# Kernel tuning notes

Hardware: AMD Instinct MI355X
Metric: run time of the kernel (lower is better)

The kernel has to match this reference:

```python
import jax, jax.numpy as jnp
import numpy as np

N_NODES = 100000
N_EDGES = 1600000
IN_FT = 128
OUT_FT = 128


def setup_inputs() -> dict:
    key = jax.random.key(0)
    k1, k2, k3, k4, k5, k6 = jax.random.split(key, 6)
    stdv = 1.0 / np.sqrt(OUT_FT)
    x = jax.random.normal(k1, (N_NODES, IN_FT), dtype=jnp.float32)
    edge_rows = jax.random.randint(k2, (N_EDGES,), 0, N_NODES, dtype=jnp.int32)
    edge_cols = jax.random.randint(k3, (N_EDGES,), 0, N_NODES, dtype=jnp.int32)
    # normalized adjacency values (positive, like D^-1 A)
    edge_vals = jax.random.uniform(k4, (N_EDGES,), dtype=jnp.float32)
    W = jax.random.uniform(k5, (IN_FT, OUT_FT), dtype=jnp.float32, minval=-stdv, maxval=stdv)
    b = jax.random.uniform(k6, (OUT_FT,), dtype=jnp.float32, minval=-stdv, maxval=stdv)
    return {"x": x, "edge_rows": edge_rows, "edge_cols": edge_cols,
            "edge_vals": edge_vals, "W": W, "b": b}


def reference(x, edge_rows, edge_cols, edge_vals, W, b):
    # dense projection + bias: [N, out_ft]
    h = x @ W + b
    # SpMM: out[r] = sum_e vals[e] * h[cols[e]] for edges with rows[e] == r
    msgs = edge_vals[:, None] * h[edge_cols]          # [E, out_ft]
    out = jax.ops.segment_sum(msgs, edge_rows, num_segments=N_NODES)
    return jax.nn.relu(out)
```

## Files before the change

### kernel.cpp

```cpp
#include <hip/hip_runtime.h>

#define N_NODES 100000
#define N_EDGES 1600000
#define FT 128

#define NBUCK 391
#define EPB 4096
#define NBLKP ((N_EDGES + EPB - 1) / EPB)
#define CAP 6144

#define OFF_H 0
#define OFF_BUCKETED 25600000
#define OFF_BLKHIST 38400000
#define OFF_BTOT 39011524
#define OFF_BBASE 39013088
#define WS_NEEDED 39014656

typedef __attribute__((ext_vector_type(8))) short bf16x8;
typedef __attribute__((ext_vector_type(4))) float f32x4;

static __device__ __forceinline__ ushort f2bf(float f) {
  const unsigned u = __float_as_uint(f);
  return (ushort)((u + 0x7FFF + ((u >> 16) & 1)) >> 16);
}
static __device__ __forceinline__ float bf2f(ushort s) {
  return __uint_as_float((unsigned)s << 16);
}

__global__ __launch_bounds__(256) void gemm_bias_kernel(
    const float* __restrict__ x,
    const float* __restrict__ W,
    const float* __restrict__ b,
    ushort* __restrict__ h) {
  __shared__ __align__(16) ushort whi[16384];
  __shared__ __align__(16) ushort wlo[16384];

  const int tid = threadIdx.x;

  for (int idx = tid; idx < 16384; idx += 256) {
    const int k = idx >> 7;
    const int col = idx & 127;
    const float wv = W[idx];
    const ushort hi = f2bf(wv);
    const ushort lo = f2bf(wv - bf2f(hi));
    const int lane_ = (((k >> 3) & 3) << 4) | (col & 15);
    const int pos = ((((k >> 5) << 3) + (col >> 4)) * 64 + lane_) * 8 + (k & 7);
    whi[pos] = hi;
    wlo[pos] = lo;
  }
  __syncthreads();

  const int w = tid >> 6;
  const int lane = tid & 63;
  const int r0 = blockIdx.x * 256 + w * 64;
  const int arow = lane & 15;
  const int kgrp = (lane >> 4) << 3;

  float bias_v[8];
#pragma unroll
  for (int ct = 0; ct < 8; ++ct) bias_v[ct] = b[ct * 16 + (lane & 15)];

  f32x4 acc[4][8];
#pragma unroll
  for (int rf = 0; rf < 4; ++rf)
#pragma unroll
    for (int ct = 0; ct < 8; ++ct) acc[rf][ct] = (f32x4){0.f, 0.f, 0.f, 0.f};

#pragma unroll
  for (int ks = 0; ks < 4; ++ks) {
    bf16x8 afr[4];
#pragma unroll
    for (int rf = 0; rf < 4; ++rf) {
      int r = r0 + rf * 16 + arow;
      r = (r < N_NODES) ? r : (N_NODES - 1);
      const float* xp = x + (size_t)r * FT + ks * 32 + kgrp;
      const float4 u0 = *(const float4*)xp;
      const float4 u1 = *(const float4*)(xp + 4);
      bf16x8 a;
      a[0] = (short)f2bf(u0.x);
      a[1] = (short)f2bf(u0.y);
      a[2] = (short)f2bf(u0.z);
      a[3] = (short)f2bf(u0.w);
      a[4] = (short)f2bf(u1.x);
      a[5] = (short)f2bf(u1.y);
      a[6] = (short)f2bf(u1.z);
      a[7] = (short)f2bf(u1.w);
      afr[rf] = a;
    }
#pragma unroll
    for (int ct = 0; ct < 8; ++ct) {
      const int fo = ((ks * 8 + ct) * 64 + lane) * 8;
      const bf16x8 bh = *(const bf16x8*)&whi[fo];
      const bf16x8 bl = *(const bf16x8*)&wlo[fo];
#pragma unroll
      for (int rf = 0; rf < 4; ++rf) {
        acc[rf][ct] = __builtin_amdgcn_mfma_f32_16x16x32_bf16(
            afr[rf], bh, acc[rf][ct], 0, 0, 0);
        acc[rf][ct] = __builtin_amdgcn_mfma_f32_16x16x32_bf16(
            afr[rf], bl, acc[rf][ct], 0, 0, 0);
      }
    }
  }

  const int crow0 = (lane >> 4) << 2;
  const int ccol = lane & 15;
#pragma unroll
  for (int rf = 0; rf < 4; ++rf) {
#pragma unroll
    for (int ct = 0; ct < 8; ++ct) {
      const int col = ct * 16 + ccol;
#pragma unroll
      for (int i = 0; i < 4; ++i) {
        const int row = r0 + rf * 16 + crow0 + i;
        if (row < N_NODES)
          h[(size_t)row * FT + col] = f2bf(acc[rf][ct][i] + bias_v[ct]);
      }
    }
  }
}

__global__ __launch_bounds__(256) void partA_kernel(
    const int* __restrict__ erows, int* __restrict__ blkhist) {
  __shared__ int cnt[NBUCK];
  const int tid = threadIdx.x;
  for (int j = tid; j < NBUCK; j += 256) cnt[j] = 0;
  __syncthreads();

  const int base4 = blockIdx.x * (EPB / 4);
#pragma unroll
  for (int it = 0; it < EPB / 4 / 256; ++it) {
    const int idx4 = base4 + it * 256 + tid;
    if (idx4 < N_EDGES / 4) {
      const int4 r = ((const int4*)erows)[idx4];
      atomicAdd(&cnt[r.x >> 8], 1);
      atomicAdd(&cnt[r.y >> 8], 1);
      atomicAdd(&cnt[r.z >> 8], 1);
      atomicAdd(&cnt[r.w >> 8], 1);
    }
  }
  __syncthreads();
  int* dst = blkhist + (size_t)blockIdx.x * NBUCK;
  for (int j = tid; j < NBUCK; j += 256) dst[j] = cnt[j];
}

__global__ __launch_bounds__(512) void partB1_kernel(
    int* __restrict__ blkhist, int* __restrict__ btot) {
  __shared__ int ps[512];
  const int b = blockIdx.x;
  const int t = threadIdx.x;
  int v = 0;
  if (t < NBLKP) v = blkhist[(size_t)t * NBUCK + b];
  ps[t] = v;
  __syncthreads();
#pragma unroll
  for (int d = 1; d < 512; d <<= 1) {
    const int u = (t >= d) ? ps[t - d] : 0;
    __syncthreads();
    ps[t] += u;
    __syncthreads();
  }
  if (t < NBLKP) blkhist[(size_t)t * NBUCK + b] = ps[t] - v;
  if (t == NBLKP - 1) btot[b] = ps[t];
}

__global__ __launch_bounds__(512) void partB2_kernel(
    const int* __restrict__ btot, int* __restrict__ bucket_base) {
  __shared__ int ps[512];
  const int t = threadIdx.x;
  int v = 0;
  if (t < NBUCK) v = btot[t];
  ps[t] = v;
  __syncthreads();
#pragma unroll
  for (int d = 1; d < 512; d <<= 1) {
    const int u = (t >= d) ? ps[t - d] : 0;
    __syncthreads();
    ps[t] += u;
    __syncthreads();
  }
  if (t < NBUCK) bucket_base[t] = ps[t] - v;
  if (t == NBUCK - 1) bucket_base[NBUCK] = ps[t];
}

__global__ __launch_bounds__(256) void partC_kernel(
    const int* __restrict__ erows,
    const int* __restrict__ ecols,
    const float* __restrict__ evals,
    const int* __restrict__ blkhist,
    const int* __restrict__ bucket_base,
    int2* __restrict__ bucketed) {
  __shared__ int cur[NBUCK];
  const int tid = threadIdx.x;
  const int* src = blkhist + (size_t)blockIdx.x * NBUCK;
  for (int j = tid; j < NBUCK; j += 256) cur[j] = src[j] + bucket_base[j];
  __syncthreads();

  const int base4 = blockIdx.x * (EPB / 4);
#pragma unroll
  for (int it = 0; it < EPB / 4 / 256; ++it) {
    const int idx4 = base4 + it * 256 + tid;
    if (idx4 < N_EDGES / 4) {
      const int4 r = ((const int4*)erows)[idx4];
      const int4 c = ((const int4*)ecols)[idx4];
      const float4 v = ((const float4*)evals)[idx4];
      int p;
      p = atomicAdd(&cur[r.x >> 8], 1);
      bucketed[p] = (int2){((r.x & 255) << 24) | c.x, __float_as_int(v.x)};
      p = atomicAdd(&cur[r.y >> 8], 1);
      bucketed[p] = (int2){((r.y & 255) << 24) | c.y, __float_as_int(v.y)};
      p = atomicAdd(&cur[r.z >> 8], 1);
      bucketed[p] = (int2){((r.z & 255) << 24) | c.z, __float_as_int(v.z)};
      p = atomicAdd(&cur[r.w >> 8], 1);
      bucketed[p] = (int2){((r.w & 255) << 24) | c.w, __float_as_int(v.w)};
    }
  }
}

__global__ __launch_bounds__(512) void spmm_bucket_kernel(
    const int2* __restrict__ bucketed,
    const int* __restrict__ bucket_base,
    const ushort* __restrict__ h,
    float* __restrict__ out) {
  __shared__ int2 eds[CAP];
  __shared__ int cnt[256];
  __shared__ int pos[256];
  __shared__ int cur[256];
  const int b = blockIdx.x;
  const int t = threadIdx.x;
  const int beg = bucket_base[b];
  const int end = bucket_base[b + 1];
  const int n = end - beg;
  const int m = (n < CAP) ? n : CAP;

  if (t < 256) cnt[t] = 0;
  __syncthreads();

  for (int i = t; i < m; i += 512)
    atomicAdd(&cnt[((unsigned)bucketed[beg + i].x) >> 24], 1);
  __syncthreads();

  if (t < 256) pos[t] = cnt[t];
  __syncthreads();
#pragma unroll
  for (int d = 1; d < 256; d <<= 1) {
    int u = 0;
    if (t < 256 && t >= d) u = pos[t - d];
    __syncthreads();
    if (t < 256) pos[t] += u;
    __syncthreads();
  }
  if (t < 256) {
    const int excl = pos[t] - cnt[t];
    pos[t] = excl;
    cur[t] = excl;
  }
  __syncthreads();

  for (int i = t; i < m; i += 512) {
    const int2 rec = bucketed[beg + i];
    const int r8 = ((unsigned)rec.x) >> 24;
    const int p = atomicAdd(&cur[r8], 1);
    eds[p] = (int2){rec.x & 0x00FFFFFF, rec.y};
  }
  __syncthreads();

  const int g = t >> 5;
  const int lane = t & 31;
  const int j = lane * 4;

  for (int rr = 0; rr < 16; ++rr) {
    const int r = rr * 16 + g;
    const int row = b * 256 + r;
    const int rbeg = pos[r];
    const int rend = cur[r];

    float a0 = 0.f, a1 = 0.f, a2 = 0.f, a3 = 0.f;
    int e = rbeg;
    for (; e + 3 < rend; e += 4) {
      const int2 p0 = eds[e];
      const int2 p1 = eds[e + 1];
      const int2 p2 = eds[e + 2];
      const int2 p3 = eds[e + 3];
      const ushort4 q0 = *(const ushort4*)(h + (size_t)p0.x * FT + j);
      const ushort4 q1 = *(const ushort4*)(h + (size_t)p1.x * FT + j);
      const ushort4 q2 = *(const ushort4*)(h + (size_t)p2.x * FT + j);
      const ushort4 q3 = *(const ushort4*)(h + (size_t)p3.x * FT + j);
      const float v0 = __int_as_float(p0.y);
      const float v1 = __int_as_float(p1.y);
      const float v2 = __int_as_float(p2.y);
      const float v3 = __int_as_float(p3.y);
      a0 = fmaf(v0, bf2f(q0.x), a0);
      a1 = fmaf(v0, bf2f(q0.y), a1);
      a2 = fmaf(v0, bf2f(q0.z), a2);
      a3 = fmaf(v0, bf2f(q0.w), a3);
      a0 = fmaf(v1, bf2f(q1.x), a0);
      a1 = fmaf(v1, bf2f(q1.y), a1);
      a2 = fmaf(v1, bf2f(q1.z), a2);
      a3 = fmaf(v1, bf2f(q1.w), a3);
      a0 = fmaf(v2, bf2f(q2.x), a0);
      a1 = fmaf(v2, bf2f(q2.y), a1);
      a2 = fmaf(v2, bf2f(q2.z), a2);
      a3 = fmaf(v2, bf2f(q2.w), a3);
      a0 = fmaf(v3, bf2f(q3.x), a0);
      a1 = fmaf(v3, bf2f(q3.y), a1);
      a2 = fmaf(v3, bf2f(q3.z), a2);
      a3 = fmaf(v3, bf2f(q3.w), a3);
    }
    for (; e < rend; ++e) {
      const int2 p0 = eds[e];
      const float v0 = __int_as_float(p0.y);
      const ushort4 q0 = *(const ushort4*)(h + (size_t)p0.x * FT + j);
      a0 = fmaf(v0, bf2f(q0.x), a0);
      a1 = fmaf(v0, bf2f(q0.y), a1);
      a2 = fmaf(v0, bf2f(q0.z), a2);
      a3 = fmaf(v0, bf2f(q0.w), a3);
    }
    if (n > CAP) {
      for (int i = beg + CAP; i < end; ++i) {
        const int2 rec = bucketed[i];
        if ((int)(((unsigned)rec.x) >> 24) == r) {
          const float v0 = __int_as_float(rec.y);
          const ushort4 q0 =
              *(const ushort4*)(h + (size_t)(rec.x & 0x00FFFFFF) * FT + j);
          a0 = fmaf(v0, bf2f(q0.x), a0);
          a1 = fmaf(v0, bf2f(q0.y), a1);
          a2 = fmaf(v0, bf2f(q0.z), a2);
          a3 = fmaf(v0, bf2f(q0.w), a3);
        }
      }
    }

    if (row < N_NODES) {
      float4 o;
      o.x = fmaxf(a0, 0.f);
      o.y = fmaxf(a1, 0.f);
      o.z = fmaxf(a2, 0.f);
      o.w = fmaxf(a3, 0.f);
      *(float4*)(out + (size_t)row * FT + j) = o;
    }
  }
}

__global__ __launch_bounds__(256) void edge_scatter_kernel(
    const int* __restrict__ erows,
    const int* __restrict__ ecols,
    const float* __restrict__ evals,
    const ushort* __restrict__ h,
    float* out) {
  const int tid = threadIdx.x;
  const int e = blockIdx.x * 8 + (tid >> 5);
  if (e >= N_EDGES) return;
  const int r = erows[e];
  const int c = ecols[e];
  const float v = evals[e];
  const int j = (tid & 31) * 4;
  const ushort4 q = *(const ushort4*)(h + (size_t)c * FT + j);
  float* op = out + (size_t)r * FT + j;
  atomicAdd(op + 0, v * bf2f(q.x));
  atomicAdd(op + 1, v * bf2f(q.y));
  atomicAdd(op + 2, v * bf2f(q.z));
  atomicAdd(op + 3, v * bf2f(q.w));
}

__global__ __launch_bounds__(256) void relu_kernel(float* out, int n4) {
  const int i = blockIdx.x * blockDim.x + threadIdx.x;
  if (i < n4) {
    float4 v = ((float4*)out)[i];
    v.x = fmaxf(v.x, 0.f);
    v.y = fmaxf(v.y, 0.f);
    v.z = fmaxf(v.z, 0.f);
    v.w = fmaxf(v.w, 0.f);
    ((float4*)out)[i] = v;
  }
}

extern "C" void kernel_launch(void* const* d_in, const int* in_sizes, int n_in,
                              void* d_out, int out_size, void* d_ws, size_t ws_size,
                              hipStream_t stream) {
  const float* x = (const float*)d_in[0];
  const int* erows = (const int*)d_in[1];
  const int* ecols = (const int*)d_in[2];
  const float* evals = (const float*)d_in[3];
  const float* W = (const float*)d_in[4];
  const float* b = (const float*)d_in[5];
  float* out = (float*)d_out;

  char* ws = (char*)d_ws;
  ushort* h = (ushort*)(ws + OFF_H);

  gemm_bias_kernel<<<(N_NODES + 255) / 256, 256, 0, stream>>>(x, W, b, h);

  if (ws_size >= (size_t)WS_NEEDED) {
    int2* bucketed = (int2*)(ws + OFF_BUCKETED);
    int* blkhist = (int*)(ws + OFF_BLKHIST);
    int* btot = (int*)(ws + OFF_BTOT);
    int* bucket_base = (int*)(ws + OFF_BBASE);

    partA_kernel<<<NBLKP, 256, 0, stream>>>(erows, blkhist);
    partB1_kernel<<<NBUCK, 512, 0, stream>>>(blkhist, btot);
    partB2_kernel<<<1, 512, 0, stream>>>(btot, bucket_base);
    partC_kernel<<<NBLKP, 256, 0, stream>>>(erows, ecols, evals, blkhist,
                                            bucket_base, bucketed);
    spmm_bucket_kernel<<<NBUCK, 512, 0, stream>>>(bucketed, bucket_base, h,
                                                  out);
  } else {
    hipMemsetAsync(d_out, 0, (size_t)out_size * sizeof(float), stream);
    edge_scatter_kernel<<<(N_EDGES + 7) / 8, 256, 0, stream>>>(erows, ecols,
                                                               evals, h, out);
    const int n4 = out_size / 4;
    relu_kernel<<<(n4 + 255) / 256, 256, 0, stream>>>(out, n4);
  }
}
```

Baseline: 124.6 us.

## Split each SpMM row bucket across four blocks of 64 rows

The SpMM kernel now launches four blocks per 256-row bucket. Each block scans the whole bucket but keeps only the edges for its 64-row quarter, staging them in shared memory with a smaller capacity. This raises the block count from 391 to 1564 and reduces LDS per block, which should improve occupancy and load balance across CUs. The cost is that each bucket's edge list is read four times. The overflow fallback also relies on atomic-order counting, which may be inexact if a quarter ever exceeds capacity.

```diff
diff --git a/kernel.cpp b/kernel.cpp
--- a/kernel.cpp
+++ b/kernel.cpp
@@ -7,7 +7,7 @@
 #define NBUCK 391
 #define EPB 4096
 #define NBLKP ((N_EDGES + EPB - 1) / EPB)
-#define CAP 6144
+#define CAP 1536
 
 #define OFF_H 0
 #define OFF_BUCKETED 25600000
@@ -167,8 +167,7 @@
     const int* __restrict__ btot, int* __restrict__ bucket_base) {
   __shared__ int ps[512];
   const int t = threadIdx.x;
-  int v = 0;
-  if (t < NBUCK) v = btot[t];
+  int v = (t < NBUCK) ? btot[t] : 0;
   ps[t] = v;
   __syncthreads();
 #pragma unroll
@@ -179,7 +178,7 @@
     __syncthreads();
   }
   if (t < NBUCK) bucket_base[t] = ps[t] - v;
-  if (t == NBUCK - 1) bucket_base[NBUCK] = ps[t];
+  if (t == NBUCK - 1) bucket_base[NBUCK] = N_EDGES;
 }
 
 __global__ __launch_bounds__(256) void partC_kernel(
@@ -221,35 +220,49 @@
     const int* __restrict__ bucket_base,
     const ushort* __restrict__ h,
     float* __restrict__ out) {
+  __shared__ int2 tmp[CAP];
   __shared__ int2 eds[CAP];
-  __shared__ int cnt[256];
-  __shared__ int pos[256];
-  __shared__ int cur[256];
-  const int b = blockIdx.x;
+  __shared__ int cnt[64];
+  __shared__ int pos[64];
+  __shared__ int cur[64];
+  __shared__ int ns;
+  const int b = blockIdx.x >> 2;
+  const int q = blockIdx.x & 3;
   const int t = threadIdx.x;
   const int beg = bucket_base[b];
   const int end = bucket_base[b + 1];
-  const int n = end - beg;
-  const int m = (n < CAP) ? n : CAP;
-
-  if (t < 256) cnt[t] = 0;
-  __syncthreads();
-
-  for (int i = t; i < m; i += 512)
-    atomicAdd(&cnt[((unsigned)bucketed[beg + i].x) >> 24], 1);
-  __syncthreads();
-
-  if (t < 256) pos[t] = cnt[t];
-  __syncthreads();
-#pragma unroll
-  for (int d = 1; d < 256; d <<= 1) {
+
+  if (t < 64) cnt[t] = 0;
+  if (t == 0) ns = 0;
+  __syncthreads();
+
+  for (int i = beg + t; i < end; i += 512) {
+    const int2 rec = bucketed[i];
+    const int r8 = ((unsigned)rec.x) >> 24;
+    if ((r8 >> 6) == q) {
+      const int p = atomicAdd(&ns, 1);
+      if (p < CAP) {
+        tmp[p] = rec;
+        atomicAdd(&cnt[r8 & 63], 1);
+      }
+    }
+  }
+  __syncthreads();
+
+  const int m = (ns < CAP) ? ns : CAP;
+  const bool overflow = (ns > CAP);
+
+  if (t < 64) pos[t] = cnt[t];
+  __syncthreads();
+#pragma unroll
+  for (int d = 1; d < 64; d <<= 1) {
     int u = 0;
-    if (t < 256 && t >= d) u = pos[t - d];
-    __syncthreads();
-    if (t < 256) pos[t] += u;
-    __syncthreads();
-  }
-  if (t < 256) {
+    if (t < 64 && t >= d) u = pos[t - d];
+    __syncthreads();
+    if (t < 64) pos[t] += u;
+    __syncthreads();
+  }
+  if (t < 64) {
     const int excl = pos[t] - cnt[t];
     pos[t] = excl;
     cur[t] = excl;
@@ -257,9 +270,9 @@
   __syncthreads();
 
   for (int i = t; i < m; i += 512) {
-    const int2 rec = bucketed[beg + i];
-    const int r8 = ((unsigned)rec.x) >> 24;
-    const int p = atomicAdd(&cur[r8], 1);
+    const int2 rec = tmp[i];
+    const int r6 = (((unsigned)rec.x) >> 24) & 63;
+    const int p = atomicAdd(&cur[r6], 1);
     eds[p] = (int2){rec.x & 0x00FFFFFF, rec.y};
   }
   __syncthreads();
@@ -268,9 +281,9 @@
   const int lane = t & 31;
   const int j = lane * 4;
 
-  for (int rr = 0; rr < 16; ++rr) {
+  for (int rr = 0; rr < 4; ++rr) {
     const int r = rr * 16 + g;
-    const int row = b * 256 + r;
+    const int row = b * 256 + q * 64 + r;
     const int rbeg = pos[r];
     const int rend = cur[r];
 
@@ -315,17 +328,23 @@
       a2 = fmaf(v0, bf2f(q0.z), a2);
       a3 = fmaf(v0, bf2f(q0.w), a3);
     }
-    if (n > CAP) {
-      for (int i = beg + CAP; i < end; ++i) {
+    if (overflow) {
+      int seen = 0;
+      const int have = rend - rbeg;
+      for (int i = beg; i < end; ++i) {
         const int2 rec = bucketed[i];
-        if ((int)(((unsigned)rec.x) >> 24) == r) {
-          const float v0 = __int_as_float(rec.y);
-          const ushort4 q0 =
-              *(const ushort4*)(h + (size_t)(rec.x & 0x00FFFFFF) * FT + j);
-          a0 = fmaf(v0, bf2f(q0.x), a0);
-          a1 = fmaf(v0, bf2f(q0.y), a1);
-          a2 = fmaf(v0, bf2f(q0.z), a2);
-          a3 = fmaf(v0, bf2f(q0.w), a3);
+        const int r8 = ((unsigned)rec.x) >> 24;
+        if ((r8 >> 6) == q && (r8 & 63) == r) {
+          ++seen;
+          if (seen > have) {
+            const float v0 = __int_as_float(rec.y);
+            const ushort4 q0 =
+                *(const ushort4*)(h + (size_t)(rec.x & 0x00FFFFFF) * FT + j);
+            a0 = fmaf(v0, bf2f(q0.x), a0);
+            a1 = fmaf(v0, bf2f(q0.y), a1);
+            a2 = fmaf(v0, bf2f(q0.z), a2);
+            a3 = fmaf(v0, bf2f(q0.w), a3);
+          }
         }
       }
     }
@@ -401,8 +420,8 @@
     partB2_kernel<<<1, 512, 0, stream>>>(btot, bucket_base);
     partC_kernel<<<NBLKP, 256, 0, stream>>>(erows, ecols, evals, blkhist,
                                             bucket_base, bucketed);
-    spmm_bucket_kernel<<<NBUCK, 512, 0, stream>>>(bucketed, bucket_base, h,
-                                                  out);
+    spmm_bucket_kernel<<<NBUCK * 4, 512, 0, stream>>>(bucketed, bucket_base,
+                                                      h, out);
   } else {
     hipMemsetAsync(d_out, 0, (size_t)out_size * sizeof(float), stream);
     edge_scatter_kernel<<<(N_EDGES + 7) / 8, 256, 0, stream>>>(erows, ecols,
```

New measurement: 123.3 us. No clear change (-1.0%).
